# Optimization experiments

Hardware: AMD Instinct MI355X
Metric: run time of the kernel (lower is better)

Reference implementation:

```python
import jax, jax.numpy as jnp
import numpy as np

D = 2  # spatial dimension


def _conv_contract(image, filt, in_k, out_k):
    """Tensor convolution + contraction on a torus.
    image: (in_c, N, N) + (D,)*in_k
    filt:  (out_c, in_c, M, M) + (D,)*in_k + (D,)*out_k
    out:   (out_c, N, N) + (D,)*out_k
    Image tensor indices contract with the first in_k filter tensor indices.
    """
    in_c, N = image.shape[0], image.shape[1]
    out_c, M = filt.shape[0], filt.shape[2]
    di, do = D ** in_k, D ** out_k
    # fold tensor indices into channels: (1, in_c*di, N, N)
    img = jnp.transpose(image.reshape(in_c, N, N, di), (0, 3, 1, 2)).reshape(1, in_c * di, N, N)
    # filter -> (out_c*do, in_c*di, M, M), ordering (out_c, out_idx, in_c, in_idx)
    f = filt.reshape(out_c, in_c, M, M, di, do)
    f = jnp.transpose(f, (0, 5, 1, 4, 2, 3)).reshape(out_c * do, in_c * di, M, M)
    p = M // 2
    img = jnp.pad(img, ((0, 0), (0, 0), (p, p), (p, p)), mode='wrap')  # torus
    out = jax.lax.conv_general_dilated(
        img, f, window_strides=(1, 1), padding='VALID',
        dimension_numbers=('NCHW', 'OIHW', 'NCHW'))[0]
    out = jnp.transpose(out.reshape(out_c, do, N, N), (0, 2, 3, 1))
    return out.reshape((out_c, N, N) + (D,) * out_k)


def _synth(w, fils):
    # (out_c, in_c, n) x (n, M, M, tensor...) -> (out_c, in_c, M, M, tensor...)
    return jnp.einsum('oik,k...->oi...', w, fils)


def setup_inputs() -> dict:
    key = jax.random.key(0)
    ks = jax.random.split(key, 11)
    r = lambda k, s: jax.random.normal(k, s, dtype=jnp.float32)
    return {
        'x0': r(ks[0], (64, 256, 256)),
        'x1': r(ks[1], (64, 256, 256, 2)),
        'fil0': r(ks[2], (3, 3, 3)),
        'fil1': r(ks[3], (6, 3, 3, 2)),
        'fil2': r(ks[4], (12, 3, 3, 2, 2)),
        'w00': r(ks[5], (64, 64, 3)) * (1.0 / np.sqrt(64 * 3)),
        'w01': r(ks[6], (64, 64, 6)) * (1.0 / np.sqrt(64 * 6)),
        'w10': r(ks[7], (64, 64, 6)) * (1.0 / np.sqrt(64 * 6)),
        'w11': r(ks[8], (64, 64, 12)) * (1.0 / np.sqrt(64 * 12)),
        'b0': r(ks[9], (64, 1, 1)) * 0.05,
        'b1': r(ks[10], (64, 1, 1, 1)) * 0.05,
    }


def reference(x0, x1, fil0, fil1, fil2, w00, w01, w10, w11, b0, b1):
    # accumulate over input blocks for each target (out_k, out_p=0)
    out0 = _conv_contract(x0, _synth(w00, fil0), 0, 0) \
         + _conv_contract(x1, _synth(w10, fil1), 1, 0)
    out1 = _conv_contract(x0, _synth(w01, fil1), 0, 1) \
         + _conv_contract(x1, _synth(w11, fil2), 1, 1)
    # use_bias='auto': plain bias for scalars, mean-scaled bias for tensors
    out0 = out0 + b0
    mean1 = jnp.mean(out1, axis=(1, 2), keepdims=True)  # spatial mean
    out1 = out1 + mean1 * b1
    return (out0, out1)
```

## Files before the change

kernel.cpp:

```cpp
#include <hip/hip_runtime.h>
#include <hip/hip_bf16.h>
#include <string.h>


#define NN 256
#define NPIX 65536
#define OUT1_OFF 4194304
#define FS 160

typedef __attribute__((ext_vector_type(8))) short short8;
typedef __attribute__((ext_vector_type(4))) float floatx4;

__device__ __forceinline__ unsigned short f2b(float x) {
    unsigned int u; memcpy(&u, &x, 4);
    return (unsigned short)((u + 0x7FFFu + ((u >> 16) & 1u)) >> 16);
}
__device__ __forceinline__ float b2f16(unsigned short u) {
    unsigned int v = ((unsigned int)u) << 16; float f; memcpy(&f, &v, 4); return f;
}
__device__ __forceinline__ unsigned int pack2(float a, float b) {
    return (unsigned int)f2b(a) | ((unsigned int)f2b(b) << 16);
}

__global__ __launch_bounds__(256) void prep_kernel(const float* __restrict__ x0,
                                                   const float* __restrict__ x1,
                                                   unsigned short* __restrict__ Xb,
                                                   float* __restrict__ partial) {
    const int t = threadIdx.x;
    const int w = t >> 6, tx = t & 63;
    const int y = blockIdx.x * 4 + w;
    const int c = blockIdx.y;
    const int col0 = tx * 4;

    unsigned int u[4][8];
    float sum[16];
    if (c < 4) {
        #pragma unroll
        for (int j = 0; j < 8; j++) {
            const float4 a = *(const float4*)(x0 + (size_t)(16 * c + 2 * j) * NPIX + y * NN + col0);
            const float4 b = *(const float4*)(x0 + (size_t)(16 * c + 2 * j + 1) * NPIX + y * NN + col0);
            u[0][j] = pack2(a.x, b.x);
            u[1][j] = pack2(a.y, b.y);
            u[2][j] = pack2(a.z, b.z);
            u[3][j] = pack2(a.w, b.w);
            sum[2 * j]     = a.x + a.y + a.z + a.w;
            sum[2 * j + 1] = b.x + b.y + b.z + b.w;
        }
    } else {
        #pragma unroll
        for (int j = 0; j < 8; j++) {
            int i = 8 * (c - 4) + j;
            const float* base = x1 + ((size_t)(i * 256 + y) * 256 + col0) * 2;
            const float4 p0 = *(const float4*)(base);
            const float4 p1 = *(const float4*)(base + 4);
            u[0][j] = pack2(p0.x, p0.y);
            u[1][j] = pack2(p0.z, p0.w);
            u[2][j] = pack2(p1.x, p1.y);
            u[3][j] = pack2(p1.z, p1.w);
            sum[2 * j]     = p0.x + p0.z + p1.x + p1.z;
            sum[2 * j + 1] = p0.y + p0.w + p1.y + p1.w;
        }
    }
    uint4* dst = (uint4*)(Xb + (((size_t)y * 12 + c) * 256 + col0) * 16);
    #pragma unroll
    for (int cc = 0; cc < 4; cc++) {
        dst[cc * 2]     = make_uint4(u[cc][0], u[cc][1], u[cc][2], u[cc][3]);
        dst[cc * 2 + 1] = make_uint4(u[cc][4], u[cc][5], u[cc][6], u[cc][7]);
    }
    #pragma unroll
    for (int cl = 0; cl < 16; cl++)
        #pragma unroll
        for (int d = 1; d < 64; d <<= 1) sum[cl] += __shfl_xor(sum[cl], d, 64);
    if (tx < 16) partial[(c * 16 + tx) * 256 + y] = sum[tx];
}

__global__ void synth_kernel(const float* __restrict__ fil0, const float* __restrict__ fil1,
                             const float* __restrict__ fil2,
                             const float* __restrict__ w00, const float* __restrict__ w01,
                             const float* __restrict__ w10, const float* __restrict__ w11,
                             unsigned short* __restrict__ Fb) {
    int idx = blockIdx.x * 256 + threadIdx.x;
    if (idx >= 12 * 192 * FS) return;
    int kpos = idx % FS;
    int co   = (idx / FS) % 192;
    int c    = idx / (FS * 192);
    int tap = kpos >> 4, cl = kpos & 15;
    float s = 0.0f;
    if (tap < 9) {
        int cin = c * 16 + cl;
        if (co < 64) {
            if (cin < 64) {
                for (int k = 0; k < 3; k++)
                    s += w00[(co * 64 + cin) * 3 + k] * fil0[k * 9 + tap];
            } else {
                int i = (cin - 64) >> 1, t = (cin - 64) & 1;
                for (int k = 0; k < 6; k++)
                    s += w10[(co * 64 + i) * 6 + k] * fil1[(k * 9 + tap) * 2 + t];
            }
        } else {
            int o = (co - 64) >> 1, u = (co - 64) & 1;
            if (cin < 64) {
                for (int k = 0; k < 6; k++)
                    s += w01[(o * 64 + cin) * 6 + k] * fil1[(k * 9 + tap) * 2 + u];
            } else {
                int i = (cin - 64) >> 1, t = (cin - 64) & 1;
                for (int k = 0; k < 12; k++)
                    s += w11[(o * 64 + i) * 12 + k] * fil2[((k * 9 + tap) * 2 + t) * 2 + u];
            }
        }
    }
    Fb[idx] = f2b(s);
}

__global__ void meanbx_kernel(const unsigned short* __restrict__ Fb,
                              const float* __restrict__ partial,
                              const float* __restrict__ b1, float* __restrict__ meanb) {
    __shared__ float mX[192];
    __shared__ float rd[4];
    const int c1 = blockIdx.x;
    const int t = threadIdx.x;
    if (t < 192) {
        const float4* p = (const float4*)(partial + (size_t)t * 256);
        float s = 0.0f;
        for (int j = 0; j < 64; j++) { float4 v = p[j]; s += v.x + v.y + v.z + v.w; }
        mX[t] = s * (1.0f / 65536.0f);
    }
    __syncthreads();
    float s = 0.0f;
    for (int e = t; e < 1728; e += 256) {
        int c = e / 144, r = e - c * 144;
        int tap = r >> 4, cl = r & 15;
        s += b2f16(Fb[((size_t)c * 192 + 64 + c1) * FS + tap * 16 + cl]) * mX[c * 16 + cl];
    }
#pragma unroll
    for (int d = 1; d < 64; d <<= 1) s += __shfl_xor(s, d, 64);
    if ((t & 63) == 0) rd[t >> 6] = s;
    __syncthreads();
    if (t == 0) meanb[c1] = (rd[0] + rd[1] + rd[2] + rd[3]) * b1[c1 >> 1];
}

__global__ __launch_bounds__(512, 4) void conv_kernel(
    const unsigned short* __restrict__ Xb, const unsigned short* __restrict__ Fb,
    const float* __restrict__ b0, const float* __restrict__ meanb,
    float* __restrict__ out) {

    __shared__ __align__(16) unsigned short Flds[96 * FS];
    __shared__ __align__(16) unsigned short Xlds[3 * 256 * 16];

    const int tid = threadIdx.x;
    const int y = blockIdx.x;
    const int m0 = blockIdx.y * 96;
    const int l = tid & 63, w = tid >> 6;
    const int wm = w >> 2, wn = w & 3;
    const int mw = wm * 48, nw = wn * 64;
    const int ln = l & 15, quad = l >> 4;

    int baseA[3];
#pragma unroll
    for (int f = 0; f < 3; f++) baseA[f] = (mw + f * 16 + ln) * FS + quad * 8;
    int cb[4];
#pragma unroll
    for (int g = 0; g < 4; g++) cb[g] = nw + g * 16 + ln;
    int rofs[5], dxv[5];
#pragma unroll
    for (int ks = 0; ks < 5; ks++) {
        int tap = 2 * ks + (quad >> 1);
        int r, dx;
        if (tap > 8) { r = 0; dx = 0; }
        else { r = tap / 3; dx = tap - 3 * r - 1; }
        rofs[ks] = r * 4096 + (quad & 1) * 8;
        dxv[ks] = dx;
    }

    floatx4 acc[3][4];
#pragma unroll
    for (int f = 0; f < 3; f++)
#pragma unroll
        for (int g = 0; g < 4; g++) acc[f][g] = (floatx4){0.f, 0.f, 0.f, 0.f};

    for (int c = 0; c < 12; c++) {
        const unsigned short* FbC = Fb + ((size_t)c * 192 + m0) * FS;
        for (int s = w; s < 54; s += 8) {
            const unsigned short* g;
            unsigned short* lb;
            if (s < 30) {
                g = FbC + s * 512;
                lb = Flds + s * 512;
            } else {
                int j = s - 30;
                int r = j >> 3, p = j & 7;
                int yr = (y + r + 255) & 255;
                g = Xb + (((size_t)yr * 12 + c) * 4096) + p * 512;
                lb = Xlds + r * 4096 + p * 512;
            }
            __builtin_amdgcn_global_load_lds(
                (const __attribute__((address_space(1))) unsigned int*)(g + l * 8),
                (__attribute__((address_space(3))) unsigned int*)lb, 16, 0, 0);
        }
        __syncthreads();

#pragma unroll
        for (int ks = 0; ks < 5; ks++) {
            short8 A[3], B[4];
#pragma unroll
            for (int f = 0; f < 3; f++)
                A[f] = *(const short8*)(Flds + baseA[f] + ks * 32);
#pragma unroll
            for (int g = 0; g < 4; g++) {
                int colw = (cb[g] + dxv[ks]) & 255;
                B[g] = *(const short8*)(Xlds + rofs[ks] + colw * 16);
            }
#pragma unroll
            for (int f = 0; f < 3; f++)
#pragma unroll
                for (int g = 0; g < 4; g++)
                    acc[f][g] = __builtin_amdgcn_mfma_f32_16x16x32_bf16(A[f], B[g], acc[f][g], 0, 0, 0);
        }
        __syncthreads();
    }

#pragma unroll
    for (int f = 0; f < 3; f++) {
        int cob = m0 + mw + f * 16 + quad * 4;
#pragma unroll
        for (int g = 0; g < 4; g++) {
            int col = nw + g * 16 + ln;
            if (cob < 64) {
#pragma unroll
                for (int reg = 0; reg < 4; reg++)
                    out[(size_t)(cob + reg) * NPIX + y * NN + col] = acc[f][g][reg] + b0[cob + reg];
            } else {
#pragma unroll
                for (int reg = 0; reg < 4; reg += 2) {
                    int c1 = cob + reg - 64;
                    int o = c1 >> 1;
                    float2 v = make_float2(acc[f][g][reg] + meanb[c1],
                                           acc[f][g][reg + 1] + meanb[c1 + 1]);
                    *((float2*)(out + OUT1_OFF) + ((size_t)o * NPIX + y * NN + col)) = v;
                }
            }
        }
    }
}

extern "C" void kernel_launch(void* const* d_in, const int* in_sizes, int n_in,
                              void* d_out, int out_size, void* d_ws, size_t ws_size,
                              hipStream_t stream) {
    const float* x0   = (const float*)d_in[0];
    const float* x1   = (const float*)d_in[1];
    const float* fil0 = (const float*)d_in[2];
    const float* fil1 = (const float*)d_in[3];
    const float* fil2 = (const float*)d_in[4];
    const float* w00  = (const float*)d_in[5];
    const float* w01  = (const float*)d_in[6];
    const float* w10  = (const float*)d_in[7];
    const float* w11  = (const float*)d_in[8];
    const float* b0   = (const float*)d_in[9];
    const float* b1   = (const float*)d_in[10];

    unsigned short* Xb = (unsigned short*)d_ws;
    unsigned short* Fb = (unsigned short*)((char*)d_ws + 25165824);
    float* partial     = (float*)((char*)d_ws + 25903104);
    float* meanb       = (float*)((char*)d_ws + 26099712);
    float* out = (float*)d_out;

    prep_kernel<<<dim3(64, 12), 256, 0, stream>>>(x0, x1, Xb, partial);

    synth_kernel<<<(12 * 192 * FS + 255) / 256, 256, 0, stream>>>(
        fil0, fil1, fil2, w00, w01, w10, w11, Fb);

    meanbx_kernel<<<128, 256, 0, stream>>>(Fb, partial, b1, meanb);

    conv_kernel<<<dim3(NN, 2), 512, 0, stream>>>(Xb, Fb, b0, meanb, out);
}
```

Before: 171.7 us.

## Double-buffer conv LDS staging and XOR-swizzle filter/image layouts

```diff
diff --git a/kernel.cpp b/kernel.cpp
--- a/kernel.cpp
+++ b/kernel.cpp
@@ -6,7 +6,10 @@
 #define NN 256
 #define NPIX 65536
 #define OUT1_OFF 4194304
-#define FS 160
+#define FS 192
+#define FBYT 36864
+#define XBYT 24576
+#define BUFB 61440
 
 typedef __attribute__((ext_vector_type(8))) short short8;
 typedef __attribute__((ext_vector_type(4))) float floatx4;
@@ -61,11 +64,13 @@
             sum[2 * j + 1] = p0.y + p0.w + p1.y + p1.w;
         }
     }
-    uint4* dst = (uint4*)(Xb + (((size_t)y * 12 + c) * 256 + col0) * 16);
+    char* rowp = (char*)(Xb + ((size_t)y * 12 + c) * 4096);
     #pragma unroll
     for (int cc = 0; cc < 4; cc++) {
-        dst[cc * 2]     = make_uint4(u[cc][0], u[cc][1], u[cc][2], u[cc][3]);
-        dst[cc * 2 + 1] = make_uint4(u[cc][4], u[cc][5], u[cc][6], u[cc][7]);
+        int col = col0 + cc;
+        int sw = ((col >> 3) & 7) << 4;
+        *(uint4*)(rowp + ((col * 32)      ^ sw)) = make_uint4(u[cc][0], u[cc][1], u[cc][2], u[cc][3]);
+        *(uint4*)(rowp + ((col * 32 + 16) ^ sw)) = make_uint4(u[cc][4], u[cc][5], u[cc][6], u[cc][7]);
     }
     #pragma unroll
     for (int cl = 0; cl < 16; cl++)
@@ -109,7 +114,7 @@
             }
         }
     }
-    Fb[idx] = f2b(s);
+    Fb[((size_t)c * 192 + co) * FS + (kpos ^ ((co & 7) << 3))] = f2b(s);
 }
 
 __global__ void meanbx_kernel(const unsigned short* __restrict__ Fb,
@@ -130,7 +135,8 @@
     for (int e = t; e < 1728; e += 256) {
         int c = e / 144, r = e - c * 144;
         int tap = r >> 4, cl = r & 15;
-        s += b2f16(Fb[((size_t)c * 192 + 64 + c1) * FS + tap * 16 + cl]) * mX[c * 16 + cl];
+        s += b2f16(Fb[((size_t)c * 192 + 64 + c1) * FS + ((tap * 16 + cl) ^ ((c1 & 7) << 3))])
+             * mX[c * 16 + cl];
     }
 #pragma unroll
     for (int d = 1; d < 64; d <<= 1) s += __shfl_xor(s, d, 64);
@@ -139,13 +145,12 @@
     if (t == 0) meanb[c1] = (rd[0] + rd[1] + rd[2] + rd[3]) * b1[c1 >> 1];
 }
 
-__global__ __launch_bounds__(512, 4) void conv_kernel(
+__global__ __launch_bounds__(512, 2) void conv_kernel(
     const unsigned short* __restrict__ Xb, const unsigned short* __restrict__ Fb,
     const float* __restrict__ b0, const float* __restrict__ meanb,
     float* __restrict__ out) {
 
-    __shared__ __align__(16) unsigned short Flds[96 * FS];
-    __shared__ __align__(16) unsigned short Xlds[3 * 256 * 16];
+    __shared__ __align__(16) char lds[2 * BUFB];
 
     const int tid = threadIdx.x;
     const int y = blockIdx.x;
@@ -155,21 +160,26 @@
     const int mw = wm * 48, nw = wn * 64;
     const int ln = l & 15, quad = l >> 4;
 
-    int baseA[3];
-#pragma unroll
-    for (int f = 0; f < 3; f++) baseA[f] = (mw + f * 16 + ln) * FS + quad * 8;
-    int cb[4];
-#pragma unroll
-    for (int g = 0; g < 4; g++) cb[g] = nw + g * 16 + ln;
-    int rofs[5], dxv[5];
+    int addrA[5][3];
+    int addrB[5][4];
+    const int swzA = (ln & 7) << 4;
 #pragma unroll
     for (int ks = 0; ks < 5; ks++) {
+#pragma unroll
+        for (int f = 0; f < 3; f++) {
+            int row = mw + f * 16 + ln;
+            addrA[ks][f] = (row * (FS * 2) + quad * 16 + ks * 64) ^ swzA;
+        }
         int tap = 2 * ks + (quad >> 1);
         int r, dx;
         if (tap > 8) { r = 0; dx = 0; }
         else { r = tap / 3; dx = tap - 3 * r - 1; }
-        rofs[ks] = r * 4096 + (quad & 1) * 8;
-        dxv[ks] = dx;
+#pragma unroll
+        for (int g = 0; g < 4; g++) {
+            int colw = (nw + g * 16 + ln + dx) & 255;
+            addrB[ks][g] = FBYT + r * 8192 +
+                ((colw * 32 + (quad & 1) * 16) ^ (((colw >> 3) & 7) << 4));
+        }
     }
 
     floatx4 acc[3][4];
@@ -178,38 +188,42 @@
 #pragma unroll
         for (int g = 0; g < 4; g++) acc[f][g] = (floatx4){0.f, 0.f, 0.f, 0.f};
 
-    for (int c = 0; c < 12; c++) {
+    auto stage = [&](int c, int bsel) {
         const unsigned short* FbC = Fb + ((size_t)c * 192 + m0) * FS;
-        for (int s = w; s < 54; s += 8) {
+        char* base = lds + bsel * BUFB;
+        for (int s = w; s < 60; s += 8) {
             const unsigned short* g;
-            unsigned short* lb;
-            if (s < 30) {
+            char* lb;
+            if (s < 36) {
                 g = FbC + s * 512;
-                lb = Flds + s * 512;
-            } else {
-                int j = s - 30;
+                lb = base + s * 1024;
+            } else {
+                int j = s - 36;
                 int r = j >> 3, p = j & 7;
                 int yr = (y + r + 255) & 255;
-                g = Xb + (((size_t)yr * 12 + c) * 4096) + p * 512;
-                lb = Xlds + r * 4096 + p * 512;
+                g = Xb + ((size_t)yr * 12 + c) * 4096 + p * 512;
+                lb = base + FBYT + r * 8192 + p * 1024;
             }
             __builtin_amdgcn_global_load_lds(
                 (const __attribute__((address_space(1))) unsigned int*)(g + l * 8),
                 (__attribute__((address_space(3))) unsigned int*)lb, 16, 0, 0);
         }
-        __syncthreads();
-
+    };
+
+    stage(0, 0);
+    __syncthreads();
+
+    int cur = 0;
+    for (int c = 0; c < 12; c++) {
+        if (c < 11) stage(c + 1, cur ^ 1);
+        const char* fb = lds + cur * BUFB;
 #pragma unroll
         for (int ks = 0; ks < 5; ks++) {
             short8 A[3], B[4];
 #pragma unroll
-            for (int f = 0; f < 3; f++)
-                A[f] = *(const short8*)(Flds + baseA[f] + ks * 32);
-#pragma unroll
-            for (int g = 0; g < 4; g++) {
-                int colw = (cb[g] + dxv[ks]) & 255;
-                B[g] = *(const short8*)(Xlds + rofs[ks] + colw * 16);
-            }
+            for (int f = 0; f < 3; f++) A[f] = *(const short8*)(fb + addrA[ks][f]);
+#pragma unroll
+            for (int g = 0; g < 4; g++) B[g] = *(const short8*)(fb + addrB[ks][g]);
 #pragma unroll
             for (int f = 0; f < 3; f++)
 #pragma unroll
@@ -217,6 +231,7 @@
                     acc[f][g] = __builtin_amdgcn_mfma_f32_16x16x32_bf16(A[f], B[g], acc[f][g], 0, 0, 0);
         }
         __syncthreads();
+        cur ^= 1;
     }
 
 #pragma unroll
@@ -260,8 +275,8 @@
 
     unsigned short* Xb = (unsigned short*)d_ws;
     unsigned short* Fb = (unsigned short*)((char*)d_ws + 25165824);
-    float* partial     = (float*)((char*)d_ws + 25903104);
-    float* meanb       = (float*)((char*)d_ws + 26099712);
+    float* partial     = (float*)((char*)d_ws + 26050560);
+    float* meanb       = (float*)((char*)d_ws + 26247168);
     float* out = (float*)d_out;
 
     prep_kernel<<<dim3(64, 12), 256, 0, stream>>>(x0, x1, Xb, partial);
```

After: 187.0 us. +8.9%, slower.

## Fuse prep and synth kernels, split mean reduction, swizzle block-to-row mapping

Applied to the files above, without the earlier changes.

```diff
diff --git a/kernel.cpp b/kernel.cpp
--- a/kernel.cpp
+++ b/kernel.cpp
@@ -22,109 +22,118 @@
     return (unsigned int)f2b(a) | ((unsigned int)f2b(b) << 16);
 }
 
-__global__ __launch_bounds__(256) void prep_kernel(const float* __restrict__ x0,
-                                                   const float* __restrict__ x1,
-                                                   unsigned short* __restrict__ Xb,
-                                                   float* __restrict__ partial) {
-    const int t = threadIdx.x;
-    const int w = t >> 6, tx = t & 63;
-    const int y = blockIdx.x * 4 + w;
-    const int c = blockIdx.y;
-    const int col0 = tx * 4;
-
-    unsigned int u[4][8];
-    float sum[16];
-    if (c < 4) {
+__global__ __launch_bounds__(256) void prep_synth_kernel(
+    const float* __restrict__ x0, const float* __restrict__ x1,
+    const float* __restrict__ fil0, const float* __restrict__ fil1,
+    const float* __restrict__ fil2,
+    const float* __restrict__ w00, const float* __restrict__ w01,
+    const float* __restrict__ w10, const float* __restrict__ w11,
+    unsigned short* __restrict__ Xb, float* __restrict__ partial,
+    unsigned short* __restrict__ Fb) {
+
+    const int bid = blockIdx.x;
+    if (bid < 768) {
+        const int t = threadIdx.x;
+        const int w = t >> 6, tx = t & 63;
+        const int bxs = bid & 63;
+        const int c = bid >> 6;
+        const int yg = ((bxs & 7) << 3) | (bxs >> 3);
+        const int y = yg * 4 + w;
+        const int col0 = tx * 4;
+
+        unsigned int u[4][8];
+        float sum[16];
+        if (c < 4) {
+            #pragma unroll
+            for (int j = 0; j < 8; j++) {
+                const float4 a = *(const float4*)(x0 + (size_t)(16 * c + 2 * j) * NPIX + y * NN + col0);
+                const float4 b = *(const float4*)(x0 + (size_t)(16 * c + 2 * j + 1) * NPIX + y * NN + col0);
+                u[0][j] = pack2(a.x, b.x);
+                u[1][j] = pack2(a.y, b.y);
+                u[2][j] = pack2(a.z, b.z);
+                u[3][j] = pack2(a.w, b.w);
+                sum[2 * j]     = a.x + a.y + a.z + a.w;
+                sum[2 * j + 1] = b.x + b.y + b.z + b.w;
+            }
+        } else {
+            #pragma unroll
+            for (int j = 0; j < 8; j++) {
+                int i = 8 * (c - 4) + j;
+                const float* base = x1 + ((size_t)(i * 256 + y) * 256 + col0) * 2;
+                const float4 p0 = *(const float4*)(base);
+                const float4 p1 = *(const float4*)(base + 4);
+                u[0][j] = pack2(p0.x, p0.y);
+                u[1][j] = pack2(p0.z, p0.w);
+                u[2][j] = pack2(p1.x, p1.y);
+                u[3][j] = pack2(p1.z, p1.w);
+                sum[2 * j]     = p0.x + p0.z + p1.x + p1.z;
+                sum[2 * j + 1] = p0.y + p0.w + p1.y + p1.w;
+            }
+        }
+        uint4* dst = (uint4*)(Xb + (((size_t)y * 12 + c) * 256 + col0) * 16);
         #pragma unroll
-        for (int j = 0; j < 8; j++) {
-            const float4 a = *(const float4*)(x0 + (size_t)(16 * c + 2 * j) * NPIX + y * NN + col0);
-            const float4 b = *(const float4*)(x0 + (size_t)(16 * c + 2 * j + 1) * NPIX + y * NN + col0);
-            u[0][j] = pack2(a.x, b.x);
-            u[1][j] = pack2(a.y, b.y);
-            u[2][j] = pack2(a.z, b.z);
-            u[3][j] = pack2(a.w, b.w);
-            sum[2 * j]     = a.x + a.y + a.z + a.w;
-            sum[2 * j + 1] = b.x + b.y + b.z + b.w;
-        }
+        for (int cc = 0; cc < 4; cc++) {
+            dst[cc * 2]     = make_uint4(u[cc][0], u[cc][1], u[cc][2], u[cc][3]);
+            dst[cc * 2 + 1] = make_uint4(u[cc][4], u[cc][5], u[cc][6], u[cc][7]);
+        }
+        #pragma unroll
+        for (int cl = 0; cl < 16; cl++)
+            #pragma unroll
+            for (int d = 1; d < 64; d <<= 1) sum[cl] += __shfl_xor(sum[cl], d, 64);
+        if (tx < 16) partial[(c * 16 + tx) * 256 + y] = sum[tx];
     } else {
-        #pragma unroll
-        for (int j = 0; j < 8; j++) {
-            int i = 8 * (c - 4) + j;
-            const float* base = x1 + ((size_t)(i * 256 + y) * 256 + col0) * 2;
-            const float4 p0 = *(const float4*)(base);
-            const float4 p1 = *(const float4*)(base + 4);
-            u[0][j] = pack2(p0.x, p0.y);
-            u[1][j] = pack2(p0.z, p0.w);
-            u[2][j] = pack2(p1.x, p1.y);
-            u[3][j] = pack2(p1.z, p1.w);
-            sum[2 * j]     = p0.x + p0.z + p1.x + p1.z;
-            sum[2 * j + 1] = p0.y + p0.w + p1.y + p1.w;
-        }
-    }
-    uint4* dst = (uint4*)(Xb + (((size_t)y * 12 + c) * 256 + col0) * 16);
-    #pragma unroll
-    for (int cc = 0; cc < 4; cc++) {
-        dst[cc * 2]     = make_uint4(u[cc][0], u[cc][1], u[cc][2], u[cc][3]);
-        dst[cc * 2 + 1] = make_uint4(u[cc][4], u[cc][5], u[cc][6], u[cc][7]);
-    }
-    #pragma unroll
-    for (int cl = 0; cl < 16; cl++)
-        #pragma unroll
-        for (int d = 1; d < 64; d <<= 1) sum[cl] += __shfl_xor(sum[cl], d, 64);
-    if (tx < 16) partial[(c * 16 + tx) * 256 + y] = sum[tx];
-}
-
-__global__ void synth_kernel(const float* __restrict__ fil0, const float* __restrict__ fil1,
-                             const float* __restrict__ fil2,
-                             const float* __restrict__ w00, const float* __restrict__ w01,
-                             const float* __restrict__ w10, const float* __restrict__ w11,
-                             unsigned short* __restrict__ Fb) {
-    int idx = blockIdx.x * 256 + threadIdx.x;
-    if (idx >= 12 * 192 * FS) return;
-    int kpos = idx % FS;
-    int co   = (idx / FS) % 192;
-    int c    = idx / (FS * 192);
-    int tap = kpos >> 4, cl = kpos & 15;
-    float s = 0.0f;
-    if (tap < 9) {
-        int cin = c * 16 + cl;
-        if (co < 64) {
-            if (cin < 64) {
-                for (int k = 0; k < 3; k++)
-                    s += w00[(co * 64 + cin) * 3 + k] * fil0[k * 9 + tap];
+        int idx = (bid - 768) * 256 + threadIdx.x;
+        if (idx >= 12 * 192 * FS) return;
+        int kpos = idx % FS;
+        int co   = (idx / FS) % 192;
+        int c    = idx / (FS * 192);
+        int tap = kpos >> 4, cl = kpos & 15;
+        float s = 0.0f;
+        if (tap < 9) {
+            int cin = c * 16 + cl;
+            if (co < 64) {
+                if (cin < 64) {
+                    for (int k = 0; k < 3; k++)
+                        s += w00[(co * 64 + cin) * 3 + k] * fil0[k * 9 + tap];
+                } else {
+                    int i = (cin - 64) >> 1, t = (cin - 64) & 1;
+                    for (int k = 0; k < 6; k++)
+                        s += w10[(co * 64 + i) * 6 + k] * fil1[(k * 9 + tap) * 2 + t];
+                }
             } else {
-                int i = (cin - 64) >> 1, t = (cin - 64) & 1;
-                for (int k = 0; k < 6; k++)
-                    s += w10[(co * 64 + i) * 6 + k] * fil1[(k * 9 + tap) * 2 + t];
-            }
-        } else {
-            int o = (co - 64) >> 1, u = (co - 64) & 1;
-            if (cin < 64) {
-                for (int k = 0; k < 6; k++)
-                    s += w01[(o * 64 + cin) * 6 + k] * fil1[(k * 9 + tap) * 2 + u];
-            } else {
-                int i = (cin - 64) >> 1, t = (cin - 64) & 1;
-                for (int k = 0; k < 12; k++)
-                    s += w11[(o * 64 + i) * 12 + k] * fil2[((k * 9 + tap) * 2 + t) * 2 + u];
-            }
-        }
-    }
-    Fb[idx] = f2b(s);
+                int o = (co - 64) >> 1, u = (co - 64) & 1;
+                if (cin < 64) {
+                    for (int k = 0; k < 6; k++)
+                        s += w01[(o * 64 + cin) * 6 + k] * fil1[(k * 9 + tap) * 2 + u];
+                } else {
+                    int i = (cin - 64) >> 1, t = (cin - 64) & 1;
+                    for (int k = 0; k < 12; k++)
+                        s += w11[(o * 64 + i) * 12 + k] * fil2[((k * 9 + tap) * 2 + t) * 2 + u];
+                }
+            }
+        }
+        Fb[idx] = f2b(s);
+    }
+}
+
+__global__ void meanx_kernel(const float* __restrict__ partial, float* __restrict__ mXg) {
+    const int cc = blockIdx.x;
+    const int l = threadIdx.x;
+    float4 v = ((const float4*)(partial + (size_t)cc * 256))[l];
+    float s = v.x + v.y + v.z + v.w;
+#pragma unroll
+    for (int d = 1; d < 64; d <<= 1) s += __shfl_xor(s, d, 64);
+    if (l == 0) mXg[cc] = s * (1.0f / 65536.0f);
 }
 
 __global__ void meanbx_kernel(const unsigned short* __restrict__ Fb,
-                              const float* __restrict__ partial,
+                              const float* __restrict__ mXg,
                               const float* __restrict__ b1, float* __restrict__ meanb) {
     __shared__ float mX[192];
     __shared__ float rd[4];
     const int c1 = blockIdx.x;
     const int t = threadIdx.x;
-    if (t < 192) {
-        const float4* p = (const float4*)(partial + (size_t)t * 256);
-        float s = 0.0f;
-        for (int j = 0; j < 64; j++) { float4 v = p[j]; s += v.x + v.y + v.z + v.w; }
-        mX[t] = s * (1.0f / 65536.0f);
-    }
+    if (t < 192) mX[t] = mXg[t];
     __syncthreads();
     float s = 0.0f;
     for (int e = t; e < 1728; e += 256) {
@@ -148,7 +157,8 @@
     __shared__ __align__(16) unsigned short Xlds[3 * 256 * 16];
 
     const int tid = threadIdx.x;
-    const int y = blockIdx.x;
+    const int bx = blockIdx.x;
+    const int y = ((bx & 7) << 5) | (bx >> 3);
     const int m0 = blockIdx.y * 96;
     const int l = tid & 63, w = tid >> 6;
     const int wm = w >> 2, wn = w & 3;
@@ -262,14 +272,15 @@
     unsigned short* Fb = (unsigned short*)((char*)d_ws + 25165824);
     float* partial     = (float*)((char*)d_ws + 25903104);
     float* meanb       = (float*)((char*)d_ws + 26099712);
+    float* mXg         = (float*)((char*)d_ws + 26100224);
     float* out = (float*)d_out;
 
-    prep_kernel<<<dim3(64, 12), 256, 0, stream>>>(x0, x1, Xb, partial);
-
-    synth_kernel<<<(12 * 192 * FS + 255) / 256, 256, 0, stream>>>(
-        fil0, fil1, fil2, w00, w01, w10, w11, Fb);
-
-    meanbx_kernel<<<128, 256, 0, stream>>>(Fb, partial, b1, meanb);
+    prep_synth_kernel<<<768 + 1440, 256, 0, stream>>>(
+        x0, x1, fil0, fil1, fil2, w00, w01, w10, w11, Xb, partial, Fb);
+
+    meanx_kernel<<<192, 64, 0, stream>>>(partial, mXg);
+
+    meanbx_kernel<<<128, 256, 0, stream>>>(Fb, mXg, b1, meanb);
 
     conv_kernel<<<dim3(NN, 2), 512, 0, stream>>>(Xb, Fb, b0, meanb, out);
 }
```

Measured after the change: 166.2 us. -3.2%, faster.
